# Kernel optimization log

Measured on AMD Instinct MI355X. Metric: run time of the kernel, lower is better.

Reference implementation:

```python
import jax, jax.numpy as jnp
import numpy as np
import math

N_NODES = 50000
N_FEAT = 512
HIDDEN = 512
N_CLUSTERS = 16
N_EDGES = 1600000
CLUSTER_REG = 1.0


def setup_inputs() -> dict:
    key = jax.random.key(0)
    ks = jax.random.split(key, 8)
    src = jax.random.randint(ks[0], (N_EDGES,), 0, N_NODES, dtype=jnp.int32)
    dst = jax.random.randint(ks[1], (N_EDGES,), 0, N_NODES, dtype=jnp.int32)
    graph_vals = jnp.ones((N_EDGES,), dtype=jnp.float32)
    gnorm_vals = jax.random.uniform(ks[2], (N_EDGES,), dtype=jnp.float32)
    features = jax.random.normal(ks[3], (N_NODES, N_FEAT), dtype=jnp.float32)
    # GCN params (DGI-style GCN: Linear(in,out,bias=False) + bias param)
    W = jax.random.normal(ks[4], (N_FEAT, HIDDEN), dtype=jnp.float32) * (1.0 / math.sqrt(N_FEAT))
    b = jnp.zeros((HIDDEN,), dtype=jnp.float32)
    # transform: Linear(architecture, n_clusters), orthogonal-init approximated by scaled normal
    Wt = jax.random.normal(ks[5], (HIDDEN, N_CLUSTERS), dtype=jnp.float32) * (math.sqrt(2.0) / math.sqrt(HIDDEN))
    bt = jnp.zeros((N_CLUSTERS,), dtype=jnp.float32)
    return {"src": src, "dst": dst, "graph_vals": graph_vals, "gnorm_vals": gnorm_vals,
            "features": features, "W": W, "b": b, "Wt": Wt, "bt": bt}


def reference(src, dst, graph_vals, gnorm_vals, features, W, b, Wt, bt):
    N = features.shape[0]
    E = src.shape[0]  # static nnz
    K = Wt.shape[1]
    # GCN: selu(spmm(graph_normalised, X @ W) + b)   (dropout inactive in eval)
    xw = features @ W                                   # [N, H]
    prop = jax.ops.segment_sum(gnorm_vals[:, None] * xw[dst], src, num_segments=N)  # [N, H]
    gcn_out = jax.nn.selu(prop + b)
    # cluster assignments
    assignments = jax.nn.softmax(gcn_out @ Wt + bt, axis=1)  # [N, K]
    # degrees = column sums of sparse graph (torch.sparse.sum dim=0)
    degrees = jax.ops.segment_sum(graph_vals, dst, num_segments=N)[:, None]  # [N, 1]
    # graph_pooled = (A @ S).T @ S
    As = jax.ops.segment_sum(graph_vals[:, None] * assignments[dst], src, num_segments=N)  # [N, K]
    graph_pooled = As.T @ assignments  # [K, K]
    normalizer_left = assignments.T @ degrees          # [K, 1]
    normalizer = (normalizer_left @ normalizer_left.T) / 2.0 / E
    spectral_loss = -jnp.trace(graph_pooled - normalizer) / 2.0 / E
    cluster_sizes = jnp.sum(assignments, axis=0)       # [K]
    cluster_loss = (jnp.linalg.norm(cluster_sizes) / N * math.sqrt(float(K)) - 1.0) * CLUSTER_REG
    return spectral_loss + cluster_loss
```

## Files before the change

### kernel.cpp

```cpp
#include <hip/hip_runtime.h>
#include <math.h>

#define NN 50000
#define NF 512
#define NH 512
#define NK 16
#define NSLICE 8

typedef __attribute__((ext_vector_type(8))) short bf16x8;
typedef __attribute__((ext_vector_type(4))) float f32x4;
typedef __attribute__((ext_vector_type(2))) float f32x2;

#define RPART 128
#define TPART 2048

__device__ __forceinline__ unsigned short f2bf(float f) {
  unsigned u = __float_as_uint(f);
  unsigned r = (u + 0x7fffu + ((u >> 16) & 1u)) >> 16;
  return (unsigned short)r;
}

__global__ __launch_bounds__(256) void conv_feat(const float* __restrict__ X,
                                                 unsigned short* __restrict__ Xb, int n4) {
  for (int i = blockIdx.x * blockDim.x + threadIdx.x; i < n4; i += gridDim.x * blockDim.x) {
    float4 v = *(const float4*)(X + (size_t)i * 4);
    ushort4 o;
    o.x = f2bf(v.x); o.y = f2bf(v.y); o.z = f2bf(v.z); o.w = f2bf(v.w);
    *(ushort4*)(Xb + (size_t)i * 4) = o;
  }
}

__global__ __launch_bounds__(256) void conv_w(const float* __restrict__ W,
                                              unsigned short* __restrict__ Bp) {
  int idx = blockIdx.x * blockDim.x + threadIdx.x;
  int k = idx >> 9, col = idx & 511;
  Bp[((size_t)(k >> 3) * 512 + col) * 8 + (k & 7)] = f2bf(W[idx]);
}

#define GBM 128
#define GBN 128
#define GBK 32

__global__ __launch_bounds__(256) void gemm_bf16(const unsigned short* __restrict__ A,
                                                 const unsigned short* __restrict__ Bp,
                                                 unsigned char* __restrict__ C8,
                                                 int M, int Mpad) {
  __shared__ __align__(16) unsigned char smem[16384];
  bf16x8* Abuf = (bf16x8*)smem;
  bf16x8* Bbuf = (bf16x8*)(smem + 8192);
  const int tid = threadIdx.x;
  const int lane = tid & 63;
  const int w = tid >> 6;
  const int wr = w >> 1, wc = w & 1;
  const int bm0 = blockIdx.y * GBM;
  const int bn0 = blockIdx.x * GBN;

  f32x4 acc[4][4];
#pragma unroll
  for (int m = 0; m < 4; ++m)
#pragma unroll
    for (int n = 0; n < 4; ++n)
      acc[m][n] = (f32x4){0.f, 0.f, 0.f, 0.f};

  for (int k0 = 0; k0 < NF; k0 += GBK) {
#pragma unroll
    for (int c = 0; c < 2; ++c) {
      int slot = c * 256 + tid;
      int kc = slot >> 7;
      int rc = slot & 127;
      int gr = bm0 + rc; if (gr > M - 1) gr = M - 1;
      Abuf[slot] = *(const bf16x8*)(A + (size_t)gr * NF + k0 + kc * 8);
      int kcg = (k0 >> 3) + kc;
      Bbuf[slot] = *(const bf16x8*)(Bp + ((size_t)kcg * NH + bn0 + rc) * 8);
    }
    __syncthreads();
    bf16x8 af[4], bfr[4];
#pragma unroll
    for (int m = 0; m < 4; ++m)
      af[m] = Abuf[(lane >> 4) * 128 + wr * 64 + m * 16 + (lane & 15)];
#pragma unroll
    for (int n = 0; n < 4; ++n)
      bfr[n] = Bbuf[(lane >> 4) * 128 + wc * 64 + n * 16 + (lane & 15)];
#pragma unroll
    for (int m = 0; m < 4; ++m)
#pragma unroll
      for (int n = 0; n < 4; ++n)
        acc[m][n] = __builtin_amdgcn_mfma_f32_16x16x32_bf16(af[m], bfr[n], acc[m][n], 0, 0, 0);
    __syncthreads();
  }
#pragma unroll
  for (int m = 0; m < 4; ++m) {
    int rbase = wr * 64 + m * 16 + (lane >> 4) * 4;
#pragma unroll
    for (int n = 0; n < 4; ++n) {
      int col = wc * 64 + n * 16 + (lane & 15);
#pragma unroll
      for (int r = 0; r < 4; ++r) {
        int pk = __builtin_amdgcn_cvt_pk_fp8_f32(acc[m][n][r], 0.f, 0, false);
        smem[(rbase + r) * 128 + col] = (unsigned char)(pk & 0xFF);
      }
    }
  }
  __syncthreads();
  const int sb = bn0 >> 6;
#pragma unroll
  for (int c = 0; c < 4; ++c) {
    int id = c * 256 + tid;
    int row = id >> 3;
    int k = id & 7;
    int s = k >> 2;
    int cb = (k & 3) * 16;
    uint4 v = *(const uint4*)(smem + row * 128 + s * 64 + cb);
    *(uint4*)(C8 + ((size_t)(sb + s) * Mpad + bm0 + row) * 64 + cb) = v;
  }
}

__global__ void hist_kernel(const int* __restrict__ src, const int* __restrict__ dst,
                            const float* __restrict__ gv, int* __restrict__ counts,
                            float* __restrict__ deg, int E) {
  int e = blockIdx.x * blockDim.x + threadIdx.x;
  if (e < E) {
    atomicAdd(&counts[src[e]], 1);
    atomicAdd(&deg[dst[e]], gv[e]);
  }
}

__global__ __launch_bounds__(1024) void scan_kernel(const int* __restrict__ counts,
                                                    int* __restrict__ offs,
                                                    int* __restrict__ cursor, int n) {
  __shared__ int wsum[16];
  __shared__ int carry_sh;
  const int lane = threadIdx.x & 63;
  const int wave = threadIdx.x >> 6;
  if (threadIdx.x == 0) carry_sh = 0;
  __syncthreads();
  for (int base = 0; base < n; base += 4096) {
    int i0 = base + threadIdx.x * 4;
    int c0 = 0, c1 = 0, c2 = 0, c3 = 0;
    if (i0 + 3 < n) {
      int4 v = *(const int4*)(counts + i0);
      c0 = v.x; c1 = v.y; c2 = v.z; c3 = v.w;
    } else {
      if (i0 < n)     c0 = counts[i0];
      if (i0 + 1 < n) c1 = counts[i0 + 1];
      if (i0 + 2 < n) c2 = counts[i0 + 2];
      if (i0 + 3 < n) c3 = counts[i0 + 3];
    }
    int s = c0 + c1 + c2 + c3;
    int x = s;
#pragma unroll
    for (int d = 1; d < 64; d <<= 1) {
      int y = __shfl_up(x, d, 64);
      if (lane >= d) x += y;
    }
    if (lane == 63) wsum[wave] = x;
    __syncthreads();
    if (wave == 0 && lane < 16) {
      int w = wsum[lane];
      int xx = w;
#pragma unroll
      for (int d = 1; d < 16; d <<= 1) {
        int y = __shfl_up(xx, d, 16);
        if (lane >= d) xx += y;
      }
      wsum[lane] = xx - w;
    }
    __syncthreads();
    int exc = carry_sh + wsum[wave] + x - s;
    if (i0 < n)     { offs[i0]     = exc;                cursor[i0]     = exc; }
    if (i0 + 1 < n) { offs[i0 + 1] = exc + c0;           cursor[i0 + 1] = exc + c0; }
    if (i0 + 2 < n) { offs[i0 + 2] = exc + c0 + c1;      cursor[i0 + 2] = exc + c0 + c1; }
    if (i0 + 3 < n) { offs[i0 + 3] = exc + c0 + c1 + c2; cursor[i0 + 3] = exc + c0 + c1 + c2; }
    __syncthreads();
    if (threadIdx.x == 1023) carry_sh = carry_sh + wsum[15] + x;
    __syncthreads();
  }
  if (threadIdx.x == 0) offs[n] = carry_sh;
}

__global__ void scatter_kernel(const int* __restrict__ src, const int* __restrict__ dst,
                               const float* __restrict__ gn, int* __restrict__ cursor,
                               int2* __restrict__ epair, int E) {
  int e = blockIdx.x * blockDim.x + threadIdx.x;
  if (e < E) {
    int pos = atomicAdd(&cursor[src[e]], 1);
    int2 v; v.x = dst[e]; v.y = __float_as_int(gn[e]);
    epair[pos] = v;
  }
}

__global__ __launch_bounds__(256) void slice_kernel(const unsigned* __restrict__ xw8,
                                                    const int* __restrict__ offs,
                                                    const int2* __restrict__ epair,
                                                    const float* __restrict__ bias,
                                                    unsigned short* __restrict__ gout,
                                                    int n, int Mpad) {
  __shared__ int sk[256];
  __shared__ float sv[256];
  const int node0 = blockIdx.x * 4;
  const int slice = blockIdx.y;
  const int t = threadIdx.x;
  const int w = t >> 6;
  const int lane = t & 63;
  const int g = lane >> 4;
  const int dw = lane & 15;
  int node = node0 + w;
  int nodec = node < n ? node : n - 1;
  const int nb = offs[nodec], ne = node < n ? offs[nodec + 1] : nb;
  int last = node0 + 4 < n ? node0 + 4 : n;
  const int beg4 = offs[node0], end4 = offs[last];
  const unsigned* base = xw8 + (size_t)slice * Mpad * 16 + dw;

  float a0 = 0.f, a1 = 0.f, a2 = 0.f, a3 = 0.f;

  for (int cbeg = beg4; cbeg < end4; cbeg += 256) {
    int cend = cbeg + 256 < end4 ? cbeg + 256 : end4;
    int cnt = cend - cbeg;
    if (t < cnt) { int2 p = epair[cbeg + t]; sk[t] = p.x; sv[t] = __int_as_float(p.y); }
    __syncthreads();
    int lo = nb > cbeg ? nb : cbeg;
    int hi = ne < cend ? ne : cend;
    int e = lo + g;
    for (; e + 4 < hi; e += 8) {
      int i0 = e - cbeg, i1 = e + 4 - cbeg;
      int dn0 = sk[i0], dn1 = sk[i1];
      float g0 = sv[i0], g1 = sv[i1];
      unsigned v0 = base[(size_t)dn0 * 16];
      unsigned v1 = base[(size_t)dn1 * 16];
      f32x2 l0 = __builtin_amdgcn_cvt_pk_f32_fp8(v0, false);
      f32x2 h0 = __builtin_amdgcn_cvt_pk_f32_fp8(v0, true);
      f32x2 l1 = __builtin_amdgcn_cvt_pk_f32_fp8(v1, false);
      f32x2 h1 = __builtin_amdgcn_cvt_pk_f32_fp8(v1, true);
      a0 = fmaf(g0, l0[0], a0); a1 = fmaf(g0, l0[1], a1);
      a2 = fmaf(g0, h0[0], a2); a3 = fmaf(g0, h0[1], a3);
      a0 = fmaf(g1, l1[0], a0); a1 = fmaf(g1, l1[1], a1);
      a2 = fmaf(g1, h1[0], a2); a3 = fmaf(g1, h1[1], a3);
    }
    if (e < hi) {
      int idx = e - cbeg;
      int dn = sk[idx];
      float gval = sv[idx];
      unsigned v = base[(size_t)dn * 16];
      f32x2 l2 = __builtin_amdgcn_cvt_pk_f32_fp8(v, false);
      f32x2 h2 = __builtin_amdgcn_cvt_pk_f32_fp8(v, true);
      a0 = fmaf(gval, l2[0], a0); a1 = fmaf(gval, l2[1], a1);
      a2 = fmaf(gval, h2[0], a2); a3 = fmaf(gval, h2[1], a3);
    }
    __syncthreads();
  }

  a0 += __shfl_xor(a0, 16, 64); a1 += __shfl_xor(a1, 16, 64);
  a2 += __shfl_xor(a2, 16, 64); a3 += __shfl_xor(a3, 16, 64);
  a0 += __shfl_xor(a0, 32, 64); a1 += __shfl_xor(a1, 32, 64);
  a2 += __shfl_xor(a2, 32, 64); a3 += __shfl_xor(a3, 32, 64);

  if (g == 0 && node < n) {
    const float SC = 1.0507009873554805f, AL = 1.6732632423543772f;
    int dimb = slice * 64 + dw * 4;
    float v0 = a0 + bias[dimb + 0];
    float v1 = a1 + bias[dimb + 1];
    float v2 = a2 + bias[dimb + 2];
    float v3 = a3 + bias[dimb + 3];
    v0 = (v0 > 0.f) ? SC * v0 : SC * AL * (expf(v0) - 1.f);
    v1 = (v1 > 0.f) ? SC * v1 : SC * AL * (expf(v1) - 1.f);
    v2 = (v2 > 0.f) ? SC * v2 : SC * AL * (expf(v2) - 1.f);
    v3 = (v3 > 0.f) ? SC * v3 : SC * AL * (expf(v3) - 1.f);
    ushort4 o;
    o.x = f2bf(v0); o.y = f2bf(v1); o.z = f2bf(v2); o.w = f2bf(v3);
    *(ushort4*)(gout + (size_t)node * NH + dimb) = o;
  }
}

__global__ __launch_bounds__(256) void proj_softmax(const unsigned short* __restrict__ gout,
                                                    const float* __restrict__ Wt,
                                                    const float* __restrict__ bt,
                                                    float* __restrict__ assign, int n) {
  int node = blockIdx.x * 4 + (threadIdx.x >> 6);
  if (node >= n) return;
  int lane = threadIdx.x & 63;
  const unsigned short* row = gout + (size_t)node * NH + lane * 8;
  ushort4 u0 = *(const ushort4*)(row);
  ushort4 u1 = *(const ushort4*)(row + 4);
  float v[8];
  v[0] = __uint_as_float((unsigned)u0.x << 16);
  v[1] = __uint_as_float((unsigned)u0.y << 16);
  v[2] = __uint_as_float((unsigned)u0.z << 16);
  v[3] = __uint_as_float((unsigned)u0.w << 16);
  v[4] = __uint_as_float((unsigned)u1.x << 16);
  v[5] = __uint_as_float((unsigned)u1.y << 16);
  v[6] = __uint_as_float((unsigned)u1.z << 16);
  v[7] = __uint_as_float((unsigned)u1.w << 16);
  float p[NK];
#pragma unroll
  for (int k = 0; k < NK; ++k) p[k] = 0.f;
#pragma unroll
  for (int j = 0; j < 8; ++j) {
    const float* wr = Wt + (size_t)(lane * 8 + j) * NK;
#pragma unroll
    for (int k = 0; k < NK; ++k) p[k] = fmaf(v[j], wr[k], p[k]);
  }
#pragma unroll
  for (int off = 32; off >= 1; off >>= 1)
#pragma unroll
    for (int k = 0; k < NK; ++k) p[k] += __shfl_down(p[k], off, 64);
  if (lane == 0) {
    float l[NK], m = -1e30f;
#pragma unroll
    for (int k = 0; k < NK; ++k) { l[k] = p[k] + bt[k]; m = fmaxf(m, l[k]); }
    float s = 0.f;
#pragma unroll
    for (int k = 0; k < NK; ++k) { l[k] = expf(l[k] - m); s += l[k]; }
    float inv = 1.f / s;
    float4* arow = (float4*)(assign + (size_t)node * NK);
#pragma unroll
    for (int q = 0; q < 4; ++q)
      arow[q] = make_float4(l[q * 4] * inv, l[q * 4 + 1] * inv,
                            l[q * 4 + 2] * inv, l[q * 4 + 3] * inv);
  }
}

__global__ __launch_bounds__(256) void reduce_cs_nl(const float* __restrict__ assign,
                                                    const float* __restrict__ deg,
                                                    float* __restrict__ P1, int n) {
  __shared__ float lds[4][32];
  float cs[NK] = {}, nl[NK] = {};
  for (int i = blockIdx.x * blockDim.x + threadIdx.x; i < n; i += gridDim.x * blockDim.x) {
    float d = deg[i];
    const float4* ap = (const float4*)(assign + (size_t)i * NK);
#pragma unroll
    for (int q = 0; q < 4; ++q) {
      float4 a = ap[q];
      cs[q * 4 + 0] += a.x; cs[q * 4 + 1] += a.y;
      cs[q * 4 + 2] += a.z; cs[q * 4 + 3] += a.w;
      nl[q * 4 + 0] = fmaf(a.x, d, nl[q * 4 + 0]);
      nl[q * 4 + 1] = fmaf(a.y, d, nl[q * 4 + 1]);
      nl[q * 4 + 2] = fmaf(a.z, d, nl[q * 4 + 2]);
      nl[q * 4 + 3] = fmaf(a.w, d, nl[q * 4 + 3]);
    }
  }
#pragma unroll
  for (int off = 32; off >= 1; off >>= 1) {
#pragma unroll
    for (int k = 0; k < NK; ++k) {
      cs[k] += __shfl_down(cs[k], off, 64);
      nl[k] += __shfl_down(nl[k], off, 64);
    }
  }
  int wave = threadIdx.x >> 6, lane = threadIdx.x & 63;
  if (lane == 0) {
#pragma unroll
    for (int k = 0; k < NK; ++k) { lds[wave][k] = cs[k]; lds[wave][NK + k] = nl[k]; }
  }
  __syncthreads();
  if (threadIdx.x < 32)
    P1[(size_t)blockIdx.x * 32 + threadIdx.x] =
        lds[0][threadIdx.x] + lds[1][threadIdx.x] + lds[2][threadIdx.x] + lds[3][threadIdx.x];
}

__global__ __launch_bounds__(256) void trace_kernel(const int* __restrict__ src,
                                                    const int* __restrict__ dst,
                                                    const float* __restrict__ gv,
                                                    const float* __restrict__ assign,
                                                    float* __restrict__ T2, int E) {
  __shared__ float lds[4];
  float t = 0.f;
  for (int e = blockIdx.x * blockDim.x + threadIdx.x; e < E; e += gridDim.x * blockDim.x) {
    int s = src[e], d = dst[e];
    const float4* as = (const float4*)(assign + (size_t)s * NK);
    const float4* ad = (const float4*)(assign + (size_t)d * NK);
    float dot = 0.f;
#pragma unroll
    for (int q = 0; q < 4; ++q) {
      float4 x = as[q], y = ad[q];
      dot += x.x * y.x + x.y * y.y + x.z * y.z + x.w * y.w;
    }
    t = fmaf(gv[e], dot, t);
  }
#pragma unroll
  for (int off = 32; off >= 1; off >>= 1) t += __shfl_down(t, off, 64);
  int wave = threadIdx.x >> 6, lane = threadIdx.x & 63;
  if (lane == 0) lds[wave] = t;
  __syncthreads();
  if (threadIdx.x == 0) T2[blockIdx.x] = lds[0] + lds[1] + lds[2] + lds[3];
}

__global__ __launch_bounds__(256) void final_kernel(const float* __restrict__ P1,
                                                    const float* __restrict__ T2,
                                                    float* __restrict__ out,
                                                    int np1, int np2, int E, int n) {
  __shared__ float arr[256];
  __shared__ float csnl[32];
  const int t = threadIdx.x;
  float s = 0.f;
  for (int p = (t >> 5); p < np1; p += 8) s += P1[(size_t)p * 32 + (t & 31)];
  arr[t] = s;
  __syncthreads();
  if (t < 32) {
    float v = 0.f;
#pragma unroll
    for (int j = 0; j < 8; ++j) v += arr[t + j * 32];
    csnl[t] = v;
  }
  __syncthreads();
  float tv = 0.f;
  for (int p = t; p < np2; p += 256) tv += T2[p];
  arr[t] = tv;
  __syncthreads();
  if (t == 0) {
    float tp = 0.f;
    for (int j = 0; j < 256; ++j) tp += arr[j];
    float sc = 0.f, sn = 0.f;
#pragma unroll
    for (int k = 0; k < NK; ++k) {
      sc += csnl[k] * csnl[k];
      sn += csnl[NK + k] * csnl[NK + k];
    }
    float twoE = 2.0f * (float)E;
    float spectral = -(tp - sn / twoE) / twoE;
    float closs = (sqrtf(sc) / (float)n) * 4.0f - 1.0f;
    out[0] = spectral + closs;
  }
}

extern "C" void kernel_launch(void* const* d_in, const int* in_sizes, int n_in,
                              void* d_out, int out_size, void* d_ws, size_t ws_size,
                              hipStream_t stream) {
  const int*   src  = (const int*)d_in[0];
  const int*   dst  = (const int*)d_in[1];
  const float* gv   = (const float*)d_in[2];
  const float* gn   = (const float*)d_in[3];
  const float* feat = (const float*)d_in[4];
  const float* W    = (const float*)d_in[5];
  const float* b    = (const float*)d_in[6];
  const float* Wt   = (const float*)d_in[7];
  const float* bt   = (const float*)d_in[8];
  const int E = in_sizes[0];
  const int N = in_sizes[4] / NF;
  const int Mblocks = (N + GBM - 1) / GBM;
  const int Mpad = Mblocks * GBM;

  char* ws = (char*)d_ws;
  size_t off = 0;
  auto alloc = [&](size_t bytes) {
    void* p = ws + off;
    off += (bytes + 255) & ~(size_t)255;
    return p;
  };
  unsigned short* feat_bf = (unsigned short*)alloc((size_t)N * NF * sizeof(unsigned short));
  unsigned short* Wp      = (unsigned short*)alloc((size_t)NF * NH * sizeof(unsigned short));
  unsigned char*  xw8     = (unsigned char*)alloc((size_t)Mpad * NH);
  unsigned short* gout    = (unsigned short*)alloc((size_t)N * NH * sizeof(unsigned short));
  int*   counts = (int*)alloc((size_t)N * sizeof(int));
  int*   offs   = (int*)alloc((size_t)(N + 1) * sizeof(int));
  int*   cursor = (int*)alloc((size_t)N * sizeof(int));
  float* deg    = (float*)alloc((size_t)N * sizeof(float));
  int2*  epair  = (int2*)alloc((size_t)E * sizeof(int2));
  float* assign = (float*)alloc((size_t)N * NK * sizeof(float));
  float* P1     = (float*)alloc((size_t)RPART * 32 * sizeof(float));
  float* T2     = (float*)alloc((size_t)TPART * sizeof(float));
  (void)ws_size; (void)n_in; (void)out_size;

  hipMemsetAsync(counts, 0, (size_t)N * sizeof(int), stream);
  hipMemsetAsync(deg, 0, (size_t)N * sizeof(float), stream);

  conv_feat<<<2048, 256, 0, stream>>>(feat, feat_bf, N * NF / 4);
  conv_w<<<(NF * NH) / 256, 256, 0, stream>>>(W, Wp);

  dim3 ggrid(NH / GBN, Mblocks);
  gemm_bf16<<<ggrid, 256, 0, stream>>>(feat_bf, Wp, xw8, N, Mpad);

  int eblocks = (E + 255) / 256;
  hist_kernel<<<eblocks, 256, 0, stream>>>(src, dst, gv, counts, deg, E);
  scan_kernel<<<1, 1024, 0, stream>>>(counts, offs, cursor, N);
  scatter_kernel<<<eblocks, 256, 0, stream>>>(src, dst, gn, cursor, epair, E);

  int nblk4 = (N + 3) / 4;
  dim3 sgrid(nblk4, NSLICE);
  slice_kernel<<<sgrid, 256, 0, stream>>>((const unsigned*)xw8, offs, epair, b, gout,
                                          N, Mpad);
  proj_softmax<<<nblk4, 256, 0, stream>>>(gout, Wt, bt, assign, N);

  reduce_cs_nl<<<RPART, 256, 0, stream>>>(assign, deg, P1, N);
  trace_kernel<<<TPART, 256, 0, stream>>>(src, dst, gv, assign, T2, E);
  final_kernel<<<1, 256, 0, stream>>>(P1, T2, (float*)d_out, RPART, TPART, E, N);
}
```

Baseline: 804.4 us.

## Parallelize CSR scan, use direct-to-LDS GEMM loads, widen SpMM gathers

Replaces the single-block serial scan with a three-kernel multi-block scan (block sums, base scan, per-block scan). The GEMM tile loads now use global_load_lds to write straight into shared memory instead of going through registers. The SpMM slice kernel now has each lane gather 16 fp8 values (uint4) per edge, with 16 edges in flight per wave instead of 4. This shortens the serial scan and raises gather width, at the cost of more registers per thread and two extra kernel launches.

```diff
diff --git a/kernel.cpp b/kernel.cpp
--- a/kernel.cpp
+++ b/kernel.cpp
@@ -11,6 +11,9 @@
 typedef __attribute__((ext_vector_type(4))) float f32x4;
 typedef __attribute__((ext_vector_type(2))) float f32x2;
 
+typedef __attribute__((address_space(3))) void lds_v;
+typedef const __attribute__((address_space(1))) void gbl_v;
+
 #define RPART 128
 #define TPART 2048
 
@@ -18,6 +21,11 @@
   unsigned u = __float_as_uint(f);
   unsigned r = (u + 0x7fffu + ((u >> 16) & 1u)) >> 16;
   return (unsigned short)r;
+}
+
+__device__ __forceinline__ float selu_f(float v) {
+  const float SC = 1.0507009873554805f, AL = 1.6732632423543772f;
+  return (v > 0.f) ? SC * v : SC * AL * (expf(v) - 1.f);
 }
 
 __global__ __launch_bounds__(256) void conv_feat(const float* __restrict__ X,
@@ -50,8 +58,8 @@
   bf16x8* Bbuf = (bf16x8*)(smem + 8192);
   const int tid = threadIdx.x;
   const int lane = tid & 63;
-  const int w = tid >> 6;
-  const int wr = w >> 1, wc = w & 1;
+  const int wv = tid >> 6;
+  const int wr = wv >> 1, wc = wv & 1;
   const int bm0 = blockIdx.y * GBM;
   const int bn0 = blockIdx.x * GBN;
 
@@ -65,13 +73,16 @@
   for (int k0 = 0; k0 < NF; k0 += GBK) {
 #pragma unroll
     for (int c = 0; c < 2; ++c) {
-      int slot = c * 256 + tid;
+      int slot0 = c * 256 + wv * 64;
+      int slot = slot0 + lane;
       int kc = slot >> 7;
       int rc = slot & 127;
       int gr = bm0 + rc; if (gr > M - 1) gr = M - 1;
-      Abuf[slot] = *(const bf16x8*)(A + (size_t)gr * NF + k0 + kc * 8);
+      const unsigned short* gA = A + (size_t)gr * NF + k0 + kc * 8;
+      __builtin_amdgcn_global_load_lds((gbl_v*)gA, (lds_v*)(Abuf + slot0), 16, 0, 0);
       int kcg = (k0 >> 3) + kc;
-      Bbuf[slot] = *(const bf16x8*)(Bp + ((size_t)kcg * NH + bn0 + rc) * 8);
+      const unsigned short* gB = Bp + ((size_t)kcg * NH + bn0 + rc) * 8;
+      __builtin_amdgcn_global_load_lds((gbl_v*)gB, (lds_v*)(Bbuf + slot0), 16, 0, 0);
     }
     __syncthreads();
     bf16x8 af[4], bfr[4];
@@ -125,57 +136,76 @@
   }
 }
 
-__global__ __launch_bounds__(1024) void scan_kernel(const int* __restrict__ counts,
-                                                    int* __restrict__ offs,
-                                                    int* __restrict__ cursor, int n) {
-  __shared__ int wsum[16];
-  __shared__ int carry_sh;
-  const int lane = threadIdx.x & 63;
-  const int wave = threadIdx.x >> 6;
-  if (threadIdx.x == 0) carry_sh = 0;
-  __syncthreads();
-  for (int base = 0; base < n; base += 4096) {
-    int i0 = base + threadIdx.x * 4;
-    int c0 = 0, c1 = 0, c2 = 0, c3 = 0;
-    if (i0 + 3 < n) {
-      int4 v = *(const int4*)(counts + i0);
-      c0 = v.x; c1 = v.y; c2 = v.z; c3 = v.w;
-    } else {
-      if (i0 < n)     c0 = counts[i0];
-      if (i0 + 1 < n) c1 = counts[i0 + 1];
-      if (i0 + 2 < n) c2 = counts[i0 + 2];
-      if (i0 + 3 < n) c3 = counts[i0 + 3];
-    }
-    int s = c0 + c1 + c2 + c3;
-    int x = s;
-#pragma unroll
-    for (int d = 1; d < 64; d <<= 1) {
-      int y = __shfl_up(x, d, 64);
-      if (lane >= d) x += y;
-    }
-    if (lane == 63) wsum[wave] = x;
-    __syncthreads();
-    if (wave == 0 && lane < 16) {
-      int w = wsum[lane];
-      int xx = w;
-#pragma unroll
-      for (int d = 1; d < 16; d <<= 1) {
-        int y = __shfl_up(xx, d, 16);
-        if (lane >= d) xx += y;
-      }
-      wsum[lane] = xx - w;
-    }
-    __syncthreads();
-    int exc = carry_sh + wsum[wave] + x - s;
-    if (i0 < n)     { offs[i0]     = exc;                cursor[i0]     = exc; }
-    if (i0 + 1 < n) { offs[i0 + 1] = exc + c0;           cursor[i0 + 1] = exc + c0; }
-    if (i0 + 2 < n) { offs[i0 + 2] = exc + c0 + c1;      cursor[i0 + 2] = exc + c0 + c1; }
-    if (i0 + 3 < n) { offs[i0 + 3] = exc + c0 + c1 + c2; cursor[i0 + 3] = exc + c0 + c1 + c2; }
-    __syncthreads();
-    if (threadIdx.x == 1023) carry_sh = carry_sh + wsum[15] + x;
-    __syncthreads();
-  }
-  if (threadIdx.x == 0) offs[n] = carry_sh;
+__global__ __launch_bounds__(256) void scanA(const int* __restrict__ counts,
+                                             int* __restrict__ bsum, int n) {
+  __shared__ int ws[4];
+  int i0 = blockIdx.x * 1024 + threadIdx.x * 4;
+  int s = 0;
+  if (i0 + 3 < n) {
+    int4 v = *(const int4*)(counts + i0);
+    s = v.x + v.y + v.z + v.w;
+  } else {
+#pragma unroll
+    for (int j = 0; j < 4; ++j) if (i0 + j < n) s += counts[i0 + j];
+  }
+#pragma unroll
+  for (int off = 32; off >= 1; off >>= 1) s += __shfl_down(s, off, 64);
+  int wv = threadIdx.x >> 6, ln = threadIdx.x & 63;
+  if (ln == 0) ws[wv] = s;
+  __syncthreads();
+  if (threadIdx.x == 0) bsum[blockIdx.x] = ws[0] + ws[1] + ws[2] + ws[3];
+}
+
+__global__ __launch_bounds__(64) void scanB(const int* __restrict__ bsum,
+                                            int* __restrict__ bbase,
+                                            int* __restrict__ offs, int nb, int n) {
+  int ln = threadIdx.x;
+  int v = ln < nb ? bsum[ln] : 0;
+  int x = v;
+#pragma unroll
+  for (int d = 1; d < 64; d <<= 1) {
+    int y = __shfl_up(x, d, 64);
+    if (ln >= d) x += y;
+  }
+  if (ln < nb) bbase[ln] = x - v;
+  if (ln == nb - 1) offs[n] = x;
+}
+
+__global__ __launch_bounds__(256) void scanC(const int* __restrict__ counts,
+                                             const int* __restrict__ bbase,
+                                             int* __restrict__ offs,
+                                             int* __restrict__ cursor, int n) {
+  __shared__ int ws[4];
+  int i0 = blockIdx.x * 1024 + threadIdx.x * 4;
+  int c0 = 0, c1 = 0, c2 = 0, c3 = 0;
+  if (i0 + 3 < n) {
+    int4 v = *(const int4*)(counts + i0);
+    c0 = v.x; c1 = v.y; c2 = v.z; c3 = v.w;
+  } else {
+    if (i0 < n)     c0 = counts[i0];
+    if (i0 + 1 < n) c1 = counts[i0 + 1];
+    if (i0 + 2 < n) c2 = counts[i0 + 2];
+    if (i0 + 3 < n) c3 = counts[i0 + 3];
+  }
+  int s = c0 + c1 + c2 + c3;
+  int x = s;
+  int wv = threadIdx.x >> 6, ln = threadIdx.x & 63;
+#pragma unroll
+  for (int d = 1; d < 64; d <<= 1) {
+    int y = __shfl_up(x, d, 64);
+    if (ln >= d) x += y;
+  }
+  if (ln == 63) ws[wv] = x;
+  __syncthreads();
+  int woff = 0;
+  if (wv > 0) woff += ws[0];
+  if (wv > 1) woff += ws[1];
+  if (wv > 2) woff += ws[2];
+  int exc = bbase[blockIdx.x] + woff + x - s;
+  if (i0 < n)     { offs[i0]     = exc;                cursor[i0]     = exc; }
+  if (i0 + 1 < n) { offs[i0 + 1] = exc + c0;           cursor[i0 + 1] = exc + c0; }
+  if (i0 + 2 < n) { offs[i0 + 2] = exc + c0 + c1;      cursor[i0 + 2] = exc + c0 + c1; }
+  if (i0 + 3 < n) { offs[i0 + 3] = exc + c0 + c1 + c2; cursor[i0 + 3] = exc + c0 + c1 + c2; }
 }
 
 __global__ void scatter_kernel(const int* __restrict__ src, const int* __restrict__ dst,
@@ -189,7 +219,7 @@
   }
 }
 
-__global__ __launch_bounds__(256) void slice_kernel(const unsigned* __restrict__ xw8,
+__global__ __launch_bounds__(256) void slice_kernel(const uint4* __restrict__ xw4,
                                                     const int* __restrict__ offs,
                                                     const int2* __restrict__ epair,
                                                     const float* __restrict__ bias,
@@ -202,16 +232,25 @@
   const int t = threadIdx.x;
   const int w = t >> 6;
   const int lane = t & 63;
-  const int g = lane >> 4;
-  const int dw = lane & 15;
+  const int eg = lane >> 2;
+  const int q = lane & 3;
   int node = node0 + w;
   int nodec = node < n ? node : n - 1;
   const int nb = offs[nodec], ne = node < n ? offs[nodec + 1] : nb;
   int last = node0 + 4 < n ? node0 + 4 : n;
   const int beg4 = offs[node0], end4 = offs[last];
-  const unsigned* base = xw8 + (size_t)slice * Mpad * 16 + dw;
-
-  float a0 = 0.f, a1 = 0.f, a2 = 0.f, a3 = 0.f;
+  const size_t srow = (size_t)slice * Mpad;
+
+  float a[16];
+#pragma unroll
+  for (int j = 0; j < 16; ++j) a[j] = 0.f;
+
+#define ACCD(U, G, o) {                                               \
+    f32x2 lo_ = __builtin_amdgcn_cvt_pk_f32_fp8(U, false);            \
+    f32x2 hi_ = __builtin_amdgcn_cvt_pk_f32_fp8(U, true);             \
+    a[o+0] = fmaf(G, lo_[0], a[o+0]); a[o+1] = fmaf(G, lo_[1], a[o+1]); \
+    a[o+2] = fmaf(G, hi_[0], a[o+2]); a[o+3] = fmaf(G, hi_[1], a[o+3]); }
+#define ACC4(V, G) { ACCD((V).x, G, 0) ACCD((V).y, G, 4) ACCD((V).z, G, 8) ACCD((V).w, G, 12) }
 
   for (int cbeg = beg4; cbeg < end4; cbeg += 256) {
     int cend = cbeg + 256 < end4 ? cbeg + 256 : end4;
@@ -220,54 +259,46 @@
     __syncthreads();
     int lo = nb > cbeg ? nb : cbeg;
     int hi = ne < cend ? ne : cend;
-    int e = lo + g;
-    for (; e + 4 < hi; e += 8) {
-      int i0 = e - cbeg, i1 = e + 4 - cbeg;
+    int e = lo + eg;
+    for (; e + 16 < hi; e += 32) {
+      int i0 = e - cbeg, i1 = i0 + 16;
       int dn0 = sk[i0], dn1 = sk[i1];
       float g0 = sv[i0], g1 = sv[i1];
-      unsigned v0 = base[(size_t)dn0 * 16];
-      unsigned v1 = base[(size_t)dn1 * 16];
-      f32x2 l0 = __builtin_amdgcn_cvt_pk_f32_fp8(v0, false);
-      f32x2 h0 = __builtin_amdgcn_cvt_pk_f32_fp8(v0, true);
-      f32x2 l1 = __builtin_amdgcn_cvt_pk_f32_fp8(v1, false);
-      f32x2 h1 = __builtin_amdgcn_cvt_pk_f32_fp8(v1, true);
-      a0 = fmaf(g0, l0[0], a0); a1 = fmaf(g0, l0[1], a1);
-      a2 = fmaf(g0, h0[0], a2); a3 = fmaf(g0, h0[1], a3);
-      a0 = fmaf(g1, l1[0], a0); a1 = fmaf(g1, l1[1], a1);
-      a2 = fmaf(g1, h1[0], a2); a3 = fmaf(g1, h1[1], a3);
+      uint4 v0 = xw4[(srow + dn0) * 4 + q];
+      uint4 v1 = xw4[(srow + dn1) * 4 + q];
+      ACC4(v0, g0)
+      ACC4(v1, g1)
     }
     if (e < hi) {
       int idx = e - cbeg;
       int dn = sk[idx];
-      float gval = sv[idx];
-      unsigned v = base[(size_t)dn * 16];
-      f32x2 l2 = __builtin_amdgcn_cvt_pk_f32_fp8(v, false);
-      f32x2 h2 = __builtin_amdgcn_cvt_pk_f32_fp8(v, true);
-      a0 = fmaf(gval, l2[0], a0); a1 = fmaf(gval, l2[1], a1);
-      a2 = fmaf(gval, h2[0], a2); a3 = fmaf(gval, h2[1], a3);
+      float g = sv[idx];
+      uint4 v = xw4[(srow + dn) * 4 + q];
+      ACC4(v, g)
     }
     __syncthreads();
   }
-
-  a0 += __shfl_xor(a0, 16, 64); a1 += __shfl_xor(a1, 16, 64);
-  a2 += __shfl_xor(a2, 16, 64); a3 += __shfl_xor(a3, 16, 64);
-  a0 += __shfl_xor(a0, 32, 64); a1 += __shfl_xor(a1, 32, 64);
-  a2 += __shfl_xor(a2, 32, 64); a3 += __shfl_xor(a3, 32, 64);
-
-  if (g == 0 && node < n) {
-    const float SC = 1.0507009873554805f, AL = 1.6732632423543772f;
-    int dimb = slice * 64 + dw * 4;
-    float v0 = a0 + bias[dimb + 0];
-    float v1 = a1 + bias[dimb + 1];
-    float v2 = a2 + bias[dimb + 2];
-    float v3 = a3 + bias[dimb + 3];
-    v0 = (v0 > 0.f) ? SC * v0 : SC * AL * (expf(v0) - 1.f);
-    v1 = (v1 > 0.f) ? SC * v1 : SC * AL * (expf(v1) - 1.f);
-    v2 = (v2 > 0.f) ? SC * v2 : SC * AL * (expf(v2) - 1.f);
-    v3 = (v3 > 0.f) ? SC * v3 : SC * AL * (expf(v3) - 1.f);
-    ushort4 o;
-    o.x = f2bf(v0); o.y = f2bf(v1); o.z = f2bf(v2); o.w = f2bf(v3);
-    *(ushort4*)(gout + (size_t)node * NH + dimb) = o;
+#undef ACC4
+#undef ACCD
+
+#pragma unroll
+  for (int st = 4; st <= 32; st <<= 1) {
+#pragma unroll
+    for (int j = 0; j < 16; ++j) a[j] += __shfl_xor(a[j], st, 64);
+  }
+
+  if (eg == 0 && node < n) {
+    int dimb = slice * 64 + q * 16;
+    unsigned outw[8];
+#pragma unroll
+    for (int j = 0; j < 16; j += 2) {
+      float vA = selu_f(a[j] + bias[dimb + j]);
+      float vB = selu_f(a[j + 1] + bias[dimb + j + 1]);
+      outw[j >> 1] = (unsigned)f2bf(vA) | ((unsigned)f2bf(vB) << 16);
+    }
+    uint4* dstp = (uint4*)(gout + (size_t)node * NH + dimb);
+    dstp[0] = make_uint4(outw[0], outw[1], outw[2], outw[3]);
+    dstp[1] = make_uint4(outw[4], outw[5], outw[6], outw[7]);
   }
 }
 
@@ -313,9 +344,9 @@
     float inv = 1.f / s;
     float4* arow = (float4*)(assign + (size_t)node * NK);
 #pragma unroll
-    for (int q = 0; q < 4; ++q)
-      arow[q] = make_float4(l[q * 4] * inv, l[q * 4 + 1] * inv,
-                            l[q * 4 + 2] * inv, l[q * 4 + 3] * inv);
+    for (int qq = 0; qq < 4; ++qq)
+      arow[qq] = make_float4(l[qq * 4] * inv, l[qq * 4 + 1] * inv,
+                             l[qq * 4 + 2] * inv, l[qq * 4 + 3] * inv);
   }
 }
 
@@ -386,6 +417,7 @@
 
 __global__ __launch_bounds__(256) void final_kernel(const float* __restrict__ P1,
                                                     const float* __restrict__ T2,
+                                                    const int* __restrict__ offsn,
                                                     float* __restrict__ out,
                                                     int np1, int np2, int E, int n) {
   __shared__ float arr[256];
@@ -419,6 +451,7 @@
     float spectral = -(tp - sn / twoE) / twoE;
     float closs = (sqrtf(sc) / (float)n) * 4.0f - 1.0f;
     out[0] = spectral + closs;
+    (void)offsn;
   }
 }
 
@@ -438,6 +471,7 @@
   const int N = in_sizes[4] / NF;
   const int Mblocks = (N + GBM - 1) / GBM;
   const int Mpad = Mblocks * GBM;
+  const int nsb = (N + 1023) / 1024;
 
   char* ws = (char*)d_ws;
   size_t off = 0;
@@ -458,6 +492,8 @@
   float* assign = (float*)alloc((size_t)N * NK * sizeof(float));
   float* P1     = (float*)alloc((size_t)RPART * 32 * sizeof(float));
   float* T2     = (float*)alloc((size_t)TPART * sizeof(float));
+  int*   bsum   = (int*)alloc(64 * sizeof(int));
+  int*   bbase  = (int*)alloc(64 * sizeof(int));
   (void)ws_size; (void)n_in; (void)out_size;
 
   hipMemsetAsync(counts, 0, (size_t)N * sizeof(int), stream);
@@ -471,16 +507,18 @@
 
   int eblocks = (E + 255) / 256;
   hist_kernel<<<eblocks, 256, 0, stream>>>(src, dst, gv, counts, deg, E);
-  scan_kernel<<<1, 1024, 0, stream>>>(counts, offs, cursor, N);
+  scanA<<<nsb, 256, 0, stream>>>(counts, bsum, N);
+  scanB<<<1, 64, 0, stream>>>(bsum, bbase, offs, nsb, N);
+  scanC<<<nsb, 256, 0, stream>>>(counts, bbase, offs, cursor, N);
   scatter_kernel<<<eblocks, 256, 0, stream>>>(src, dst, gn, cursor, epair, E);
 
   int nblk4 = (N + 3) / 4;
   dim3 sgrid(nblk4, NSLICE);
-  slice_kernel<<<sgrid, 256, 0, stream>>>((const unsigned*)xw8, offs, epair, b, gout,
+  slice_kernel<<<sgrid, 256, 0, stream>>>((const uint4*)xw8, offs, epair, b, gout,
                                           N, Mpad);
   proj_softmax<<<nblk4, 256, 0, stream>>>(gout, Wt, bt, assign, N);
 
   reduce_cs_nl<<<RPART, 256, 0, stream>>>(assign, deg, P1, N);
   trace_kernel<<<TPART, 256, 0, stream>>>(src, dst, gv, assign, T2, E);
-  final_kernel<<<1, 256, 0, stream>>>(P1, T2, (float*)d_out, RPART, TPART, E, N);
-}
+  final_kernel<<<1, 256, 0, stream>>>(P1, T2, offs, (float*)d_out, RPART, TPART, E, N);
+}
```

Measured after the change: 989.4 us. 23.0% more time.
